# Kernel optimization log

Measured on AMD Instinct MI355X. Metric: run time of the kernel, lower is better.

Reference implementation:

```python
import jax, jax.numpy as jnp
import numpy as np


def conv2d(x, w, pad):
    # x: [N,C,H,W], w: [O,I,kh,kw]
    return jax.lax.conv_general_dilated(
        x, w, window_strides=(1, 1), padding=[(pad, pad), (pad, pad)],
        dimension_numbers=("NCHW", "OIHW", "NCHW"))


def group_norm1(x, g, b, eps=1e-5):
    # GroupNorm(1, C): normalize over (C,H,W) per sample, per-channel affine
    mu = jnp.mean(x, axis=(1, 2, 3), keepdims=True)
    var = jnp.mean((x - mu) ** 2, axis=(1, 2, 3), keepdims=True)
    xn = (x - mu) * jax.lax.rsqrt(var + eps)
    return xn * g[None, :, None, None] + b[None, :, None, None]


def maxpool_3x3_s2(x):
    return jax.lax.reduce_window(
        x, -jnp.inf, jax.lax.max, (1, 1, 3, 3), (1, 1, 2, 2),
        ((0, 0), (0, 0), (1, 1), (1, 1)))


def hr2o_layer(x, wq, wk, wv, wo, g, b):
    # x: [N,C,H,W]; pairwise attention over the N ROIs at each (h,w)
    q = conv2d(x, wq, 1)
    k = conv2d(x, wk, 1)
    v = conv2d(x, wv, 1)
    scale = 1.0 / jnp.sqrt(jnp.asarray(x.shape[1], x.dtype))
    # torch: (q.unsqueeze(1) * k.unsqueeze(0)).sum(2) == einsum over channels
    att = jnp.einsum("nchw,mchw->nmhw", q, k) * scale  # [N,N,H,W]
    att = jax.nn.softmax(att, axis=1)                    # softmax over keys (dim=1)
    virt = jnp.einsum("nmhw,mchw->nchw", att, v)        # [N,C,H,W]
    virt = jax.nn.relu(group_norm1(virt, g, b))
    virt = conv2d(virt, wo, 1)
    return x + virt  # dropout is identity in eval mode


def setup_inputs() -> dict:
    key = jax.random.key(0)
    ks = jax.random.split(key, 12)
    N, C_R, H, W, HID, NCLS, DEPTH = 64, 1024, 16, 16, 512, 60, 2
    s = 0.02
    return {
        "bg_feats": jax.random.normal(ks[0], (C_R, H, W), jnp.float32),
        "actor_feats": jax.random.normal(ks[1], (N, C_R), jnp.float32),
        "w_conv1": jax.random.normal(ks[2], (HID, 2 * C_R, 1, 1), jnp.float32) * s,
        "w_conv2": jax.random.normal(ks[3], (HID, HID, 3, 3), jnp.float32) * s,
        "w_q": jax.random.normal(ks[4], (DEPTH, HID, HID, 3, 3), jnp.float32) * s,
        "w_k": jax.random.normal(ks[5], (DEPTH, HID, HID, 3, 3), jnp.float32) * s,
        "w_v": jax.random.normal(ks[6], (DEPTH, HID, HID, 3, 3), jnp.float32) * s,
        "w_o": jax.random.normal(ks[7], (DEPTH, HID, HID, 3, 3), jnp.float32) * s,
        "gamma": jnp.ones((DEPTH, HID), jnp.float32),
        "beta": jnp.zeros((DEPTH, HID), jnp.float32),
        "w_fc1": jax.random.normal(ks[8], (HID, C_R), jnp.float32) * s,
        "w_fc2": jax.random.normal(ks[9], (NCLS, 2 * HID), jnp.float32) * s,
    }


def reference(bg_feats, actor_feats, w_conv1, w_conv2, w_q, w_k, w_v, w_o,
              gamma, beta, w_fc1, w_fc2):
    N = actor_feats.shape[0]
    C_R, H, W = bg_feats.shape
    # bg repeated per ROI, actor features tiled over spatial dims
    bg = jnp.broadcast_to(bg_feats[None], (N, C_R, H, W))
    tiled = jnp.broadcast_to(actor_feats[:, :, None, None], (N, C_R, H, W))
    x = jnp.concatenate([bg, tiled], axis=1)           # [N, 2*C_R, H, W]
    x = jax.nn.relu(conv2d(x, w_conv1, 0))             # 1x1 -> [N,HID,H,W]
    x = jax.nn.relu(conv2d(x, w_conv2, 0))             # 3x3 pad=0 -> H-2,W-2
    x = maxpool_3x3_s2(x)                              # -> 7x7
    for d in range(w_q.shape[0]):
        x = hr2o_layer(x, w_q[d], w_k[d], w_v[d], w_o[d], gamma[d], beta[d])
    high_order = jnp.mean(x, axis=(2, 3))              # gap -> [N,HID]
    roi = jax.nn.relu(actor_feats @ w_fc1.T)           # [N,HID]
    out = jnp.concatenate([roi, high_order], axis=1) @ w_fc2.T  # [N,num_classes]
    return out
```

## Files before the change

kernel.cpp:

```cpp
#include <hip/hip_runtime.h>
#include <math.h>


typedef __bf16 bf16x8 __attribute__((ext_vector_type(8)));
typedef float  f32x4  __attribute__((ext_vector_type(4)));

#define NROI 64
#define CR   1024
#define HIDC 512
#define NCLS 60
#define PLANE (NROI * HIDC * 49)
#define ROWH 40
#define OCALL 4608
#define TAPSTR ((size_t)OCALL * 512)
#define WL (HIDC * HIDC * 9)
#define GNCNT 25088.0f

#if defined(__has_builtin)
#  if __has_builtin(__builtin_amdgcn_global_load_lds)
#    define HAVE_GLL 1
#  endif
#endif

__device__ __forceinline__ void stage16(const void* g, void* lds_base, int lane) {
#ifdef HAVE_GLL
    __builtin_amdgcn_global_load_lds(
        (const __attribute__((address_space(1))) unsigned int*)g,
        (__attribute__((address_space(3))) unsigned int*)lds_base, 16, 0, 0);
#else
    *(uint4*)((char*)lds_base + lane * 16) = *(const uint4*)g;
#endif
}

__device__ __forceinline__ float bf2f(unsigned short h) {
    union { unsigned u; float f; } x; x.u = (unsigned)h << 16; return x.f;
}

__device__ __forceinline__ int swzkey(int r) {
    return (r & 3) ^ ((r >> 2) & 3);
}

__global__ __launch_bounds__(256) void k_misc(
    const float* __restrict__ w2, const float* __restrict__ wq,
    const float* __restrict__ wk, const float* __restrict__ wv,
    const float* __restrict__ wo, const float* __restrict__ bg,
    __bf16* __restrict__ wAll, __bf16* __restrict__ inT7,
    __bf16* __restrict__ bgT)
{
    const int b = blockIdx.x, tid = threadIdx.x;
    if (b < 4608) {
        const int bid = b;
        const float* src;
        if (bid < 512) src = w2 + (size_t)bid * 4608;
        else if (bid < 2048) {
            const int r = bid - 512;
            const float* bb = r < 512 ? wq : (r < 1024 ? wk : wv);
            src = bb + (size_t)(r & 511) * 4608;
        } else if (bid < 2560) src = wo + (size_t)(bid - 2048) * 4608;
        else if (bid < 4096) {
            const int r = bid - 2560;
            const float* bb = r < 512 ? wq : (r < 1024 ? wk : wv);
            src = bb + WL + (size_t)(r & 511) * 4608;
        } else src = wo + WL + (size_t)(bid - 4096) * 4608;
        __shared__ float s[4608];
        const float4* s4 = (const float4*)src;
        for (int i = tid; i < 1152; i += 256) ((float4*)s)[i] = s4[i];
        __syncthreads();
        unsigned* dst = (unsigned*)wAll;
        const int c = tid * 2;
        const int swz = ((c >> 3) & 3) ^ ((bid >> 1) & 3);
        const size_t cidx = (size_t)(c >> 5) * 32 + swz * 8 + (c & 7);
#pragma unroll
        for (int t = 0; t < 9; ++t) {
            const unsigned short u0 = __builtin_bit_cast(unsigned short, (__bf16)s[c * 9 + t]);
            const unsigned short u1 = __builtin_bit_cast(unsigned short, (__bf16)s[(c + 1) * 9 + t]);
            dst[((size_t)t * TAPSTR + (size_t)bid * 512 + cidx) / 2] =
                ((unsigned)u1 << 16) | u0;
        }
    } else if (b < 5120) {
        const int k = b - 4608;
        const int n = k >> 3;
        const int j0 = (k & 7) * 4;
#pragma unroll
        for (int i = 0; i < 4; ++i) {
            const int jj = j0 + i;
            int sp;
            if (jj < 9) sp = jj;
            else if (jj < 18) sp = 63 + jj;
            else { const int t = jj - 18; sp = (1 + (t >> 1)) * 9 + (t & 1) * 8; }
            unsigned* d = (unsigned*)(inT7 + ((size_t)n * 81 + sp) * 512);
            d[tid] = 0u;
        }
    } else {
        const int cb = (b - 5120) * 8;
        const int p = tid;
        bf16x8 v;
#pragma unroll
        for (int j = 0; j < 8; ++j)
            v[j] = (__bf16)bg[(size_t)(cb + j) * 256 + p];
        *(bf16x8*)(bgT + (size_t)p * 1024 + cb) = v;
    }
}

__global__ __launch_bounds__(256, 2) void k_ab(
    const __bf16* __restrict__ bgT, const float* __restrict__ actor,
    const float* __restrict__ w1, const float* __restrict__ wfc1,
    float* __restrict__ A_T, float* __restrict__ Bp, float* __restrict__ roi)
{
    const int bx = blockIdx.x, by = blockIdx.y;
    const bool isA = bx < 4;
    const bool isRoi = (bx == 5);
    const int ocWg = by * 64;
    const int tid = threadIdx.x;
    const int w = tid >> 6, lane = tid & 63;
    const int q = lane >> 4, l16 = lane & 15;

    __shared__ __align__(16) __bf16 s_a[64 * ROWH];
    __shared__ __align__(16) __bf16 s_b[64 * ROWH];

    f32x4 acc[4];
#pragma unroll
    for (int nt = 0; nt < 4; ++nt) acc[nt] = (f32x4){0.f, 0.f, 0.f, 0.f};

    const int row = tid >> 2, part = tid & 3;
    for (int ch = 0; ch < 32; ++ch) {
        const int c0 = ch * 32;
        __syncthreads();
        if (isA) {
            const uint4 vv = *(const uint4*)(
                bgT + (size_t)(bx * 64 + row) * 1024 + c0 + part * 8);
            *(uint4*)(&s_a[row * ROWH + part * 8]) = vv;
        } else {
            const float* src = actor + (size_t)row * CR + c0 + part * 8;
            bf16x8 val;
#pragma unroll
            for (int j = 0; j < 8; ++j) val[j] = (__bf16)src[j];
            *(bf16x8*)(&s_a[row * ROWH + part * 8]) = val;
        }
        {
            const float* srcb = isRoi
                ? (wfc1 + (size_t)(ocWg + row) * CR + c0 + part * 8)
                : (w1 + (size_t)(ocWg + row) * (2 * CR)
                      + (isA ? 0 : CR) + c0 + part * 8);
            bf16x8 vb;
#pragma unroll
            for (int j = 0; j < 8; ++j) vb[j] = (__bf16)srcb[j];
            *(bf16x8*)(&s_b[row * ROWH + part * 8]) = vb;
        }
        __syncthreads();
        const bf16x8 af = *(const bf16x8*)(&s_a[(w * 16 + l16) * ROWH + q * 8]);
#pragma unroll
        for (int nt = 0; nt < 4; ++nt) {
            const bf16x8 bw = *(const bf16x8*)(&s_b[(nt * 16 + l16) * ROWH + q * 8]);
            acc[nt] = __builtin_amdgcn_mfma_f32_16x16x32_bf16(af, bw, acc[nt], 0, 0, 0);
        }
    }
#pragma unroll
    for (int r = 0; r < 4; ++r) {
#pragma unroll
        for (int nt = 0; nt < 4; ++nt) {
            const int mrow = w * 16 + q * 4 + r;
            const int oc = ocWg + nt * 16 + l16;
            if (isA)       A_T[(size_t)(bx * 64 + mrow) * 512 + oc] = acc[nt][r];
            else if (isRoi) roi[(size_t)mrow * 512 + oc] = fmaxf(acc[nt][r], 0.f);
            else           Bp[(size_t)mrow * 512 + oc] = acc[nt][r];
        }
    }
}

__global__ __launch_bounds__(256) void k_prep_in2(
    const float* __restrict__ A_T, const float* __restrict__ B,
    __bf16* __restrict__ dst)
{
    const int vn = blockIdx.x;
    const int n = vn >> 2, quad = vn & 3;
    const int sp0 = blockIdx.y * 27;
    const float b0 = B[n * HIDC + threadIdx.x];
    const float b1 = B[n * HIDC + 256 + threadIdx.x];
    for (int sp = sp0; sp < sp0 + 27; ++sp) {
        const int r = sp / 9, w = sp % 9;
        const int p16 = ((quad >> 1) * 7 + r) * 16 + (quad & 1) * 7 + w;
        __bf16* d = dst + ((size_t)vn * 81 + sp) * 512;
        d[threadIdx.x]       = (__bf16)fmaxf(A_T[p16 * HIDC + threadIdx.x] + b0, 0.f);
        d[256 + threadIdx.x] = (__bf16)fmaxf(A_T[p16 * HIDC + 256 + threadIdx.x] + b1, 0.f);
    }
}

__global__ __launch_bounds__(256) void k_prep_gn(
    const float* __restrict__ virt, const float* __restrict__ statsRaw,
    const float* __restrict__ gamma, const float* __restrict__ beta,
    __bf16* __restrict__ gnT)
{
    const int vn = blockIdx.x;
    const int sp0 = blockIdx.y * 9;
    __shared__ float s_mi[2];
    if (threadIdx.x == 0) {
        const float S = statsRaw[vn * 2], Q = statsRaw[vn * 2 + 1];
        const float mean = S / GNCNT;
        s_mi[0] = mean;
        s_mi[1] = rsqrtf(Q / GNCNT - mean * mean + 1e-5f);
    }
    __syncthreads();
    const float m = s_mi[0], iv = s_mi[1];
    const int c0 = threadIdx.x, c1 = threadIdx.x + 256;
    const float g0 = gamma[c0], g1 = gamma[c1];
    const float b0 = beta[c0],  b1 = beta[c1];
    for (int sp = sp0; sp < sp0 + 9; ++sp) {
        const int rr = sp / 9, cc = sp % 9;
        __bf16* d = gnT + ((size_t)vn * 81 + sp) * 512;
        if (rr >= 1 && rr <= 7 && cc >= 1 && cc <= 7) {
            const int p = (rr - 1) * 7 + (cc - 1);
            const float* src = virt + ((size_t)vn * 49 + p) * 512;
            d[c0] = (__bf16)fmaxf((src[c0] - m) * iv * g0 + b0, 0.f);
            d[c1] = (__bf16)fmaxf((src[c1] - m) * iv * g1 + b1, 0.f);
        } else {
            d[c0] = (__bf16)0.f;
            d[c1] = (__bf16)0.f;
        }
    }
}

template<int VN, int MODE>
__global__ __launch_bounds__(256, (VN == 4) ? 2 : 3) void k_conv_pipe(
    const __bf16* __restrict__ inT,
    const __bf16* __restrict__ wAll, int ocBaseGl,
    __bf16* __restrict__ outb,
    float* __restrict__ zeroStats, float* __restrict__ gapZero,
    const float* __restrict__ resid, float* __restrict__ outf,
    __bf16* __restrict__ inT7out, float* __restrict__ gapOut)
{
    constexpr int MT = (VN == 4) ? 4 : 2;
    constexpr int SLOTS = VN * 324;
    constexpr int NSUB = (SLOTS + 255) / 256;
    constexpr int SBUF = NSUB * 256;
    constexpr int NI = NSUB / 3;
    const int tid = threadIdx.x;
    const int w = tid >> 6, lane = tid & 63;
    const int q = lane >> 4, l16 = lane & 15;
    const int vn_l = (VN == 4) ? w : (w & 1);
    const int mh   = (VN == 4) ? 0 : (w >> 1);
    const int vnBase = blockIdx.x * VN;
    const int ocWg = blockIdx.y * 64;

    if (zeroStats && blockIdx.x == 0 && blockIdx.y == 0 && tid < 128)
        zeroStats[tid] = 0.f;
    if (gapZero && blockIdx.y == 0 && blockIdx.x < 16) {
        const float4 z = {0.f, 0.f, 0.f, 0.f};
        ((float4*)gapZero)[blockIdx.x * 512 + tid * 2]     = z;
        ((float4*)gapZero)[blockIdx.x * 512 + tid * 2 + 1] = z;
    }

    __shared__ __align__(16) __bf16 s_w[2 * 3 * 2048];
    __shared__ __align__(16) __bf16 s_in[2 * SBUF * 8];

    unsigned iGo[NSUB];
#pragma unroll
    for (int s = 0; s < NSUB; ++s) {
        int idx = tid + s * 256;
        if (idx > SLOTS - 1) idx = SLOTS - 1;
        const int vnl = idx / 324, rem = idx - vnl * 324;
        const int r = rem >> 2, part = rem & 3;
        iGo[s] = (unsigned)(((vnBase + vnl) * 81 + r) * 512
                            + ((part ^ swzkey(r)) * 8));
    }
    const unsigned wGo = (unsigned)((ocBaseGl + ocWg + (tid >> 2)) * 512
                                    + (tid & 3) * 8);
    const int bOff = l16 * 32 + ((q ^ ((l16 >> 1) & 3)) << 3);

    int aLoc[MT];
#pragma unroll
    for (int mt = 0; mt < MT; ++mt) {
        int p = (mh * MT + mt) * 16 + l16;
        p = p > 48 ? 48 : p;
        aLoc[mt] = (p / 7) * 9 + (p % 7);
    }
    const int vb81 = vn_l * 81;

    f32x4 acc[MT][4];
#pragma unroll
    for (int a = 0; a < MT; ++a)
#pragma unroll
        for (int b = 0; b < 4; ++b) acc[a][b] = (f32x4){0.f, 0.f, 0.f, 0.f};

#pragma unroll
    for (int s = 0; s < NSUB; ++s)
        stage16(inT + iGo[s],
                (char*)s_in + (size_t)(s * 256 + w * 64) * 16, lane);
#pragma unroll
    for (int j = 0; j < 3; ++j)
        stage16(wAll + (size_t)j * TAPSTR + wGo,
                (char*)s_w + (size_t)j * 4096 + (size_t)w * 1024, lane);
    __syncthreads();

    for (int ch = 0; ch < 16; ++ch) {
        const int c0 = ch * 32;
        const int cur = ch & 1;
        const int nxt = cur ^ 1;
#pragma unroll
        for (int f = 0; f < 3; ++f) {
            const int P = ch * 3 + f;
            const int wpar = P & 1;
            {
                const int fn = (f == 2) ? 0 : (f + 1);
                const int cc = (f == 2) ? (c0 + 32) : c0;
#pragma unroll
                for (int j = 0; j < 3; ++j)
                    stage16(wAll + (size_t)(fn * 3 + j) * TAPSTR + wGo + cc,
                            (char*)s_w + (size_t)((wpar ^ 1) * 3 + j) * 4096
                                        + (size_t)w * 1024, lane);
            }
#pragma unroll
            for (int u = 0; u < NI; ++u) {
                const int s = f * NI + u;
                stage16(inT + iGo[s] + c0 + 32,
                        (char*)s_in + (size_t)nxt * (SBUF * 16)
                                    + (size_t)(s * 256 + w * 64) * 16, lane);
            }
            if (f == 0) {
                if constexpr (NI == 2) asm volatile("s_waitcnt vmcnt(5)" ::: "memory");
                else                   asm volatile("s_waitcnt vmcnt(4)" ::: "memory");
            } else {
                if constexpr (NI == 2) asm volatile("s_waitcnt vmcnt(7)" ::: "memory");
                else                   asm volatile("s_waitcnt vmcnt(5)" ::: "memory");
            }
            __builtin_amdgcn_sched_barrier(0);
            __builtin_amdgcn_s_barrier();
            __builtin_amdgcn_sched_barrier(0);
#pragma unroll
            for (int j = 0; j < 3; ++j) {
                const int DT = f * 9 + j;
                bf16x8 bw[4];
#pragma unroll
                for (int nt = 0; nt < 4; ++nt)
                    bw[nt] = *(const bf16x8*)(
                        &s_w[(wpar * 3 + j) * 2048 + nt * 512 + bOff]);
                bf16x8 af[MT];
#pragma unroll
                for (int mt = 0; mt < MT; ++mt) {
                    const int rl = aLoc[mt] + DT;
                    const int col = (q ^ swzkey(rl)) << 3;
                    af[mt] = *(const bf16x8*)(
                        &s_in[cur * (SBUF * 8) + (vb81 + rl) * 32 + col]);
                }
#pragma unroll
                for (int mt = 0; mt < MT; ++mt)
#pragma unroll
                    for (int nt = 0; nt < 4; ++nt)
                        acc[mt][nt] = __builtin_amdgcn_mfma_f32_16x16x32_bf16(
                            af[mt], bw[nt], acc[mt][nt], 0, 0, 0);
            }
            __builtin_amdgcn_sched_barrier(0);
            __builtin_amdgcn_s_barrier();
        }
    }

    const int vn = vnBase + vn_l;
    float gsum[4] = {0.f, 0.f, 0.f, 0.f};
#pragma unroll
    for (int mt = 0; mt < MT; ++mt) {
#pragma unroll
        for (int r = 0; r < 4; ++r) {
            const int p = (mh * MT + mt) * 16 + q * 4 + r;
            if (p >= 49) continue;
#pragma unroll
            for (int nt = 0; nt < 4; ++nt) {
                const int oc = ocWg + nt * 16 + l16;
                const float v = acc[mt][nt][r];
                if constexpr (MODE == 2) {
                    const int n = vn >> 2, quad = vn & 3;
                    const int p14 = ((quad >> 1) * 7 + p / 7) * 14 + (quad & 1) * 7 + p % 7;
                    outb[((size_t)n * 196 + p14) * 512 + oc] = (__bf16)fmaxf(v, 0.f);
                } else if constexpr (MODE == 1) {
                    const size_t addr = ((size_t)vn * 49 + p) * 512 + oc;
                    const float res = v + resid[addr];
                    if (!gapOut) outf[addr] = res;
                    gsum[nt] += res;
                    if (inT7out) {
                        const int sp = (p / 7 + 1) * 9 + (p % 7 + 1);
                        inT7out[((size_t)vn * 81 + sp) * 512 + oc] = (__bf16)res;
                    }
                } else {
                    const int conv = oc >> 9;
                    outb[(size_t)conv * PLANE + ((size_t)p * 64 + vn) * 512 + (oc & 511)]
                        = (__bf16)v;
                }
            }
        }
    }
    if constexpr (MODE == 1) {
        if (gapOut) {
#pragma unroll
            for (int nt = 0; nt < 4; ++nt)
                atomicAdd(gapOut + (size_t)vn * 512 + ocWg + nt * 16 + l16, gsum[nt]);
        }
    }
}

__global__ __launch_bounds__(256) void k_pool_prep(
    const __bf16* __restrict__ x2, __bf16* __restrict__ inT7,
    float* __restrict__ xA)
{
    const int b = blockIdx.x;
    const int n = b / 49, p = b % 49;
    const int i = p / 7, j = p % 7;
    const int sp = (i + 1) * 9 + (j + 1);
#pragma unroll
    for (int k = 0; k < 2; ++k) {
        const int c = threadIdx.x + k * 256;
        float mx = -1e30f;
#pragma unroll
        for (int di = -1; di <= 1; ++di) {
            const int rr = 2 * i + di;
            if (rr < 0 || rr >= 14) continue;
#pragma unroll
            for (int dj = -1; dj <= 1; ++dj) {
                const int cc = 2 * j + dj;
                if (cc < 0 || cc >= 14) continue;
                mx = fmaxf(mx, (float)x2[((size_t)n * 196 + rr * 14 + cc) * 512 + c]);
            }
        }
        inT7[((size_t)n * 81 + sp) * 512 + c] = (__bf16)mx;
        xA[((size_t)n * 49 + p) * 512 + c] = mx;
    }
}

__global__ __launch_bounds__(256) void k_attvirt(
    const __bf16* __restrict__ qT, const __bf16* __restrict__ kT,
    const __bf16* __restrict__ vT, float* __restrict__ virt,
    float* __restrict__ statsRaw)
{
    const int p = blockIdx.y;
    const int w = threadIdx.x >> 6, m = threadIdx.x & 63;
    const int n = blockIdx.x * 4 + w;
    __shared__ float s_q[4][HIDC];
    __shared__ float s_a[4][64];
    {
        const uint4 v = ((const uint4*)(qT + ((size_t)p * 64 + n) * HIDC))[m];
        const unsigned* u = (const unsigned*)&v;
#pragma unroll
        for (int j = 0; j < 4; ++j) {
            s_q[w][m * 8 + 2 * j]     = bf2f((unsigned short)(u[j] & 0xffff));
            s_q[w][m * 8 + 2 * j + 1] = bf2f((unsigned short)(u[j] >> 16));
        }
    }
    __syncthreads();
    const uint4* krow = (const uint4*)(kT + ((size_t)p * 64 + m) * HIDC);
    float acc0 = 0.f, acc1 = 0.f;
    for (int i = 0; i < 64; ++i) {
        const uint4 v = krow[i];
        const unsigned* u = (const unsigned*)&v;
#pragma unroll
        for (int j = 0; j < 2; ++j) {
            acc0 = fmaf(s_q[w][i * 8 + 2 * j],     bf2f((unsigned short)(u[j] & 0xffff)), acc0);
            acc0 = fmaf(s_q[w][i * 8 + 2 * j + 1], bf2f((unsigned short)(u[j] >> 16)),    acc0);
        }
#pragma unroll
        for (int j = 2; j < 4; ++j) {
            acc1 = fmaf(s_q[w][i * 8 + 2 * j],     bf2f((unsigned short)(u[j] & 0xffff)), acc1);
            acc1 = fmaf(s_q[w][i * 8 + 2 * j + 1], bf2f((unsigned short)(u[j] >> 16)),    acc1);
        }
    }
    float acc = (acc0 + acc1) * 0.044194173824159216f;
    float mx = acc;
#pragma unroll
    for (int off = 32; off; off >>= 1) mx = fmaxf(mx, __shfl_xor(mx, off));
    const float e = expf(acc - mx);
    float s = e;
#pragma unroll
    for (int off = 32; off; off >>= 1) s += __shfl_xor(s, off);
    s_a[w][m] = e / s;
    __syncthreads();
    const int c0 = m * 8;
    float av[8];
#pragma unroll
    for (int j = 0; j < 8; ++j) av[j] = 0.f;
    for (int mm = 0; mm < 64; ++mm) {
        const float a = s_a[w][mm];
        const uint4 v = *(const uint4*)(vT + ((size_t)p * 64 + mm) * HIDC + c0);
        const unsigned* u = (const unsigned*)&v;
#pragma unroll
        for (int j = 0; j < 4; ++j) {
            av[2 * j]     = fmaf(a, bf2f((unsigned short)(u[j] & 0xffff)), av[2 * j]);
            av[2 * j + 1] = fmaf(a, bf2f((unsigned short)(u[j] >> 16)),    av[2 * j + 1]);
        }
    }
    float* o = virt + ((size_t)n * 49 + p) * 512 + c0;
    float ps = 0.f, pq = 0.f;
#pragma unroll
    for (int j = 0; j < 8; ++j) {
        o[j] = av[j];
        ps += av[j];
        pq = fmaf(av[j], av[j], pq);
    }
#pragma unroll
    for (int off = 32; off; off >>= 1) {
        ps += __shfl_xor(ps, off);
        pq += __shfl_xor(pq, off);
    }
    if (m == 0) {
        atomicAdd(statsRaw + n * 2, ps);
        atomicAdd(statsRaw + n * 2 + 1, pq);
    }
}

__global__ __launch_bounds__(256) void k_final(
    const float* __restrict__ roi, const float* __restrict__ gap,
    const float* __restrict__ wfc2, float* __restrict__ out)
{
    const int n = blockIdx.x, tid = threadIdx.x;
    __shared__ float s[1024];
    s[tid]       = roi[(size_t)n * 512 + tid];
    s[tid + 256] = roi[(size_t)n * 512 + 256 + tid];
    s[tid + 512] = gap[(size_t)n * 512 + tid] * (1.f / 49.f);
    s[tid + 768] = gap[(size_t)n * 512 + 256 + tid] * (1.f / 49.f);
    __syncthreads();
    if (tid < 240) {
        const int k = tid >> 2, part = tid & 3;
        const float4* w4 = (const float4*)(wfc2 + (size_t)k * 1024 + part * 256);
        const float4* s4 = (const float4*)(s + part * 256);
        float a0 = 0.f, a1 = 0.f, a2 = 0.f, a3 = 0.f;
        for (int i = 0; i < 64; ++i) {
            const float4 wv = w4[i], sv = s4[i];
            a0 = fmaf(wv.x, sv.x, a0); a1 = fmaf(wv.y, sv.y, a1);
            a2 = fmaf(wv.z, sv.z, a2); a3 = fmaf(wv.w, sv.w, a3);
        }
        float acc = (a0 + a1) + (a2 + a3);
        acc += __shfl_xor(acc, 1);
        acc += __shfl_xor(acc, 2);
        if (part == 0) out[n * NCLS + k] = acc;
    }
}

extern "C" void kernel_launch(void* const* d_in, const int* in_sizes, int n_in,
                              void* d_out, int out_size, void* d_ws, size_t ws_size,
                              hipStream_t stream) {
    const float* bg    = (const float*)d_in[0];
    const float* actor = (const float*)d_in[1];
    const float* w1    = (const float*)d_in[2];
    const float* w2    = (const float*)d_in[3];
    const float* wq    = (const float*)d_in[4];
    const float* wk    = (const float*)d_in[5];
    const float* wv    = (const float*)d_in[6];
    const float* wo    = (const float*)d_in[7];
    const float* gamma = (const float*)d_in[8];
    const float* beta  = (const float*)d_in[9];
    const float* wfc1  = (const float*)d_in[10];
    const float* wfc2  = (const float*)d_in[11];
    float* out = (float*)d_out;
    float* ws  = (float*)d_ws;

    float* A_T   = ws;
    float* Bp    = A_T + 131072;
    float* xA    = Bp + 32768;
    float* xB    = xA + PLANE;
    float* stats = xB + PLANE;
    float* roi   = stats + 128;
    float* gap   = roi + 32768;
    float* fend  = gap + 32768;
    __bf16* x2h  = (__bf16*)fend;
    float*  virt = (float*)x2h;
    __bf16* inT2 = x2h + 6422528;
    __bf16* qkvT = inT2;
    __bf16* inT7 = inT2 + 10616832;
    __bf16* wAll = inT7 + 2654208;
    __bf16* bgT  = wAll + (size_t)9 * OCALL * 512;
    __bf16* gnT  = bgT + 262144;

    k_misc<<<5248, 256, 0, stream>>>(w2, wq, wk, wv, wo, bg, wAll, inT7, bgT);
    k_ab<<<dim3(6, 8), 256, 0, stream>>>(bgT, actor, w1, wfc1, A_T, Bp, roi);
    k_prep_in2<<<dim3(256, 3), 256, 0, stream>>>(A_T, Bp, inT2);
    k_conv_pipe<4, 2><<<dim3(64, 8), 256, 0, stream>>>(
        inT2, wAll, 0, x2h, nullptr, nullptr,
        nullptr, nullptr, nullptr, nullptr);
    k_pool_prep<<<64 * 49, 256, 0, stream>>>(x2h, inT7, xA);

    float* xin = xA;
    float* xout = xB;
    for (int d = 0; d < 2; ++d) {
        k_conv_pipe<2, 0><<<dim3(32, 24), 256, 0, stream>>>(
            inT7, wAll, 512 + d * 2048, qkvT, stats,
            d == 1 ? gap : nullptr,
            nullptr, nullptr, nullptr, nullptr);
        k_attvirt<<<dim3(16, 49), 256, 0, stream>>>(
            qkvT, qkvT + PLANE, qkvT + 2 * PLANE, virt, stats);
        k_prep_gn<<<dim3(64, 9), 256, 0, stream>>>(
            virt, stats, gamma + d * HIDC, beta + d * HIDC, gnT);
        k_conv_pipe<2, 1><<<dim3(32, 8), 256, 0, stream>>>(
            gnT, wAll, 2048 + d * 2048, nullptr, nullptr, nullptr,
            xin, xout, d == 0 ? inT7 : nullptr, d == 1 ? gap : nullptr);
        float* t = xin; xin = xout; xout = t;
    }
    k_final<<<64, 256, 0, stream>>>(roi, gap, wfc2, out);
}
```

Measured before the change: 595.4 us.

## Fuse weight conversion and first-layer GEMM into one launch, drop bgT transpose

Merges the k_misc prep kernel and the k_ab GEMM into a single k_mega launch. The first 48 blocks do the GEMM, reading bg directly with strided fp32 loads instead of going through a transposed bf16 copy, so the bgT transpose pass is removed. The weight conversion path now writes 16-byte packed stores instead of 4-byte ones. This saves a launch and lets the GEMM overlap with the conversion work, but the GEMM's bg loads become uncoalesced column gathers and its blocks share LDS sizing with the conversion blocks.

```diff
diff --git a/kernel.cpp b/kernel.cpp
--- a/kernel.cpp
+++ b/kernel.cpp
@@ -36,20 +36,89 @@
     union { unsigned u; float f; } x; x.u = (unsigned)h << 16; return x.f;
 }
 
+__device__ __forceinline__ unsigned short f2bfu(float f) {
+    return __builtin_bit_cast(unsigned short, (__bf16)f);
+}
+
 __device__ __forceinline__ int swzkey(int r) {
     return (r & 3) ^ ((r >> 2) & 3);
 }
 
-__global__ __launch_bounds__(256) void k_misc(
+__global__ __launch_bounds__(256) void k_mega(
+    const float* __restrict__ bg, const float* __restrict__ actor,
+    const float* __restrict__ w1, const float* __restrict__ wfc1,
     const float* __restrict__ w2, const float* __restrict__ wq,
     const float* __restrict__ wk, const float* __restrict__ wv,
-    const float* __restrict__ wo, const float* __restrict__ bg,
-    __bf16* __restrict__ wAll, __bf16* __restrict__ inT7,
-    __bf16* __restrict__ bgT)
+    const float* __restrict__ wo,
+    float* __restrict__ A_T, float* __restrict__ Bp, float* __restrict__ roi,
+    __bf16* __restrict__ wAll, __bf16* __restrict__ inT7)
 {
     const int b = blockIdx.x, tid = threadIdx.x;
-    if (b < 4608) {
-        const int bid = b;
+    __shared__ __align__(16) char smem[18432];
+
+    if (b < 48) {
+        const int bx = b % 6, by = b / 6;
+        const bool isA = bx < 4;
+        const bool isRoi = (bx == 5);
+        const int ocWg = by * 64;
+        const int w = tid >> 6, lane = tid & 63;
+        const int q = lane >> 4, l16 = lane & 15;
+        __bf16* s_a = (__bf16*)smem;
+        __bf16* s_b = s_a + 64 * ROWH;
+
+        f32x4 acc[4];
+#pragma unroll
+        for (int nt = 0; nt < 4; ++nt) acc[nt] = (f32x4){0.f, 0.f, 0.f, 0.f};
+
+        const int row = tid >> 2, part = tid & 3;
+        for (int ch = 0; ch < 32; ++ch) {
+            const int c0 = ch * 32;
+            __syncthreads();
+            if (isA) {
+                const int gp = bx * 64 + row;
+                bf16x8 val;
+#pragma unroll
+                for (int j = 0; j < 8; ++j)
+                    val[j] = (__bf16)bg[(size_t)(c0 + part * 8 + j) * 256 + gp];
+                *(bf16x8*)(&s_a[row * ROWH + part * 8]) = val;
+            } else {
+                const float* src = actor + (size_t)row * CR + c0 + part * 8;
+                bf16x8 val;
+#pragma unroll
+                for (int j = 0; j < 8; ++j) val[j] = (__bf16)src[j];
+                *(bf16x8*)(&s_a[row * ROWH + part * 8]) = val;
+            }
+            {
+                const float* srcb = isRoi
+                    ? (wfc1 + (size_t)(ocWg + row) * CR + c0 + part * 8)
+                    : (w1 + (size_t)(ocWg + row) * (2 * CR)
+                          + (isA ? 0 : CR) + c0 + part * 8);
+                bf16x8 vb;
+#pragma unroll
+                for (int j = 0; j < 8; ++j) vb[j] = (__bf16)srcb[j];
+                *(bf16x8*)(&s_b[row * ROWH + part * 8]) = vb;
+            }
+            __syncthreads();
+            const bf16x8 af = *(const bf16x8*)(&s_a[(w * 16 + l16) * ROWH + q * 8]);
+#pragma unroll
+            for (int nt = 0; nt < 4; ++nt) {
+                const bf16x8 bw = *(const bf16x8*)(&s_b[(nt * 16 + l16) * ROWH + q * 8]);
+                acc[nt] = __builtin_amdgcn_mfma_f32_16x16x32_bf16(af, bw, acc[nt], 0, 0, 0);
+            }
+        }
+#pragma unroll
+        for (int r = 0; r < 4; ++r) {
+#pragma unroll
+            for (int nt = 0; nt < 4; ++nt) {
+                const int mrow = w * 16 + q * 4 + r;
+                const int oc = ocWg + nt * 16 + l16;
+                if (isA)       A_T[(size_t)(bx * 64 + mrow) * 512 + oc] = acc[nt][r];
+                else if (isRoi) roi[(size_t)mrow * 512 + oc] = fmaxf(acc[nt][r], 0.f);
+                else           Bp[(size_t)mrow * 512 + oc] = acc[nt][r];
+            }
+        }
+    } else if (b < 4656) {
+        const int bid = b - 48;
         const float* src;
         if (bid < 512) src = w2 + (size_t)bid * 4608;
         else if (bid < 2048) {
@@ -62,23 +131,27 @@
             const float* bb = r < 512 ? wq : (r < 1024 ? wk : wv);
             src = bb + WL + (size_t)(r & 511) * 4608;
         } else src = wo + WL + (size_t)(bid - 4096) * 4608;
-        __shared__ float s[4608];
+        float* s = (float*)smem;
         const float4* s4 = (const float4*)src;
         for (int i = tid; i < 1152; i += 256) ((float4*)s)[i] = s4[i];
         __syncthreads();
-        unsigned* dst = (unsigned*)wAll;
-        const int c = tid * 2;
-        const int swz = ((c >> 3) & 3) ^ ((bid >> 1) & 3);
-        const size_t cidx = (size_t)(c >> 5) * 32 + swz * 8 + (c & 7);
-#pragma unroll
-        for (int t = 0; t < 9; ++t) {
-            const unsigned short u0 = __builtin_bit_cast(unsigned short, (__bf16)s[c * 9 + t]);
-            const unsigned short u1 = __builtin_bit_cast(unsigned short, (__bf16)s[(c + 1) * 9 + t]);
-            dst[((size_t)t * TAPSTR + (size_t)bid * 512 + cidx) / 2] =
-                ((unsigned)u1 << 16) | u0;
-        }
-    } else if (b < 5120) {
-        const int k = b - 4608;
+        for (int u = tid; u < 576; u += 256) {
+            const int t = u / 64, o = u - (u / 64) * 64;
+            const int swz = (o & 3) ^ ((bid >> 1) & 3);
+            const int cbase = o * 8;
+            unsigned pack[4];
+#pragma unroll
+            for (int h = 0; h < 4; ++h) {
+                const unsigned short lo = f2bfu(s[(cbase + 2 * h) * 9 + t]);
+                const unsigned short hi = f2bfu(s[(cbase + 2 * h + 1) * 9 + t]);
+                pack[h] = ((unsigned)hi << 16) | lo;
+            }
+            const size_t cidx = (size_t)(o >> 2) * 32 + (size_t)swz * 8;
+            *(uint4*)(wAll + (size_t)t * TAPSTR + (size_t)bid * 512 + cidx) =
+                *(const uint4*)pack;
+        }
+    } else {
+        const int k = b - 4656;
         const int n = k >> 3;
         const int j0 = (k & 7) * 4;
 #pragma unroll
@@ -90,80 +163,6 @@
             else { const int t = jj - 18; sp = (1 + (t >> 1)) * 9 + (t & 1) * 8; }
             unsigned* d = (unsigned*)(inT7 + ((size_t)n * 81 + sp) * 512);
             d[tid] = 0u;
-        }
-    } else {
-        const int cb = (b - 5120) * 8;
-        const int p = tid;
-        bf16x8 v;
-#pragma unroll
-        for (int j = 0; j < 8; ++j)
-            v[j] = (__bf16)bg[(size_t)(cb + j) * 256 + p];
-        *(bf16x8*)(bgT + (size_t)p * 1024 + cb) = v;
-    }
-}
-
-__global__ __launch_bounds__(256, 2) void k_ab(
-    const __bf16* __restrict__ bgT, const float* __restrict__ actor,
-    const float* __restrict__ w1, const float* __restrict__ wfc1,
-    float* __restrict__ A_T, float* __restrict__ Bp, float* __restrict__ roi)
-{
-    const int bx = blockIdx.x, by = blockIdx.y;
-    const bool isA = bx < 4;
-    const bool isRoi = (bx == 5);
-    const int ocWg = by * 64;
-    const int tid = threadIdx.x;
-    const int w = tid >> 6, lane = tid & 63;
-    const int q = lane >> 4, l16 = lane & 15;
-
-    __shared__ __align__(16) __bf16 s_a[64 * ROWH];
-    __shared__ __align__(16) __bf16 s_b[64 * ROWH];
-
-    f32x4 acc[4];
-#pragma unroll
-    for (int nt = 0; nt < 4; ++nt) acc[nt] = (f32x4){0.f, 0.f, 0.f, 0.f};
-
-    const int row = tid >> 2, part = tid & 3;
-    for (int ch = 0; ch < 32; ++ch) {
-        const int c0 = ch * 32;
-        __syncthreads();
-        if (isA) {
-            const uint4 vv = *(const uint4*)(
-                bgT + (size_t)(bx * 64 + row) * 1024 + c0 + part * 8);
-            *(uint4*)(&s_a[row * ROWH + part * 8]) = vv;
-        } else {
-            const float* src = actor + (size_t)row * CR + c0 + part * 8;
-            bf16x8 val;
-#pragma unroll
-            for (int j = 0; j < 8; ++j) val[j] = (__bf16)src[j];
-            *(bf16x8*)(&s_a[row * ROWH + part * 8]) = val;
-        }
-        {
-            const float* srcb = isRoi
-                ? (wfc1 + (size_t)(ocWg + row) * CR + c0 + part * 8)
-                : (w1 + (size_t)(ocWg + row) * (2 * CR)
-                      + (isA ? 0 : CR) + c0 + part * 8);
-            bf16x8 vb;
-#pragma unroll
-            for (int j = 0; j < 8; ++j) vb[j] = (__bf16)srcb[j];
-            *(bf16x8*)(&s_b[row * ROWH + part * 8]) = vb;
-        }
-        __syncthreads();
-        const bf16x8 af = *(const bf16x8*)(&s_a[(w * 16 + l16) * ROWH + q * 8]);
-#pragma unroll
-        for (int nt = 0; nt < 4; ++nt) {
-            const bf16x8 bw = *(const bf16x8*)(&s_b[(nt * 16 + l16) * ROWH + q * 8]);
-            acc[nt] = __builtin_amdgcn_mfma_f32_16x16x32_bf16(af, bw, acc[nt], 0, 0, 0);
-        }
-    }
-#pragma unroll
-    for (int r = 0; r < 4; ++r) {
-#pragma unroll
-        for (int nt = 0; nt < 4; ++nt) {
-            const int mrow = w * 16 + q * 4 + r;
-            const int oc = ocWg + nt * 16 + l16;
-            if (isA)       A_T[(size_t)(bx * 64 + mrow) * 512 + oc] = acc[nt][r];
-            else if (isRoi) roi[(size_t)mrow * 512 + oc] = fmaxf(acc[nt][r], 0.f);
-            else           Bp[(size_t)mrow * 512 + oc] = acc[nt][r];
         }
     }
 }
@@ -563,11 +562,10 @@
     __bf16* qkvT = inT2;
     __bf16* inT7 = inT2 + 10616832;
     __bf16* wAll = inT7 + 2654208;
-    __bf16* bgT  = wAll + (size_t)9 * OCALL * 512;
-    __bf16* gnT  = bgT + 262144;
-
-    k_misc<<<5248, 256, 0, stream>>>(w2, wq, wk, wv, wo, bg, wAll, inT7, bgT);
-    k_ab<<<dim3(6, 8), 256, 0, stream>>>(bgT, actor, w1, wfc1, A_T, Bp, roi);
+    __bf16* gnT  = wAll + (size_t)9 * OCALL * 512 + 262144;
+
+    k_mega<<<5168, 256, 0, stream>>>(bg, actor, w1, wfc1, w2, wq, wk, wv, wo,
+                                     A_T, Bp, roi, wAll, inT7);
     k_prep_in2<<<dim3(256, 3), 256, 0, stream>>>(A_T, Bp, inT2);
     k_conv_pipe<4, 2><<<dim3(64, 8), 256, 0, stream>>>(
         inT2, wAll, 0, x2h, nullptr, nullptr,
```

Result: no change. 586.5 us, median of 2 (-1.5%).
